# Optimization experiments

Hardware: AMD Instinct MI355X
Metric: run time of the kernel (lower is better)

The kernel has to match this reference:

```python
import jax, jax.numpy as jnp
import numpy as np

T, KBLK, EMB, B = 2048, 64, 512, 4


def _make_coords(t, k):
    # head1: for each j, cols = block_start(j) + arange(j % k + 1)  (block-causal local)
    j = np.arange(t)
    cnt1 = (j % k) + 1
    rows1 = np.repeat(j, cnt1)
    off1 = np.arange(cnt1.sum()) - np.repeat(np.cumsum(cnt1) - cnt1, cnt1)
    cols1 = (rows1 // k) * k + off1
    # head2: for each block start c, rows = arange(c, t), col = c  (strided block-start)
    starts = np.arange(t // k) * k
    cnt2 = t - starts
    base = np.repeat(starts, cnt2)
    off2 = np.arange(cnt2.sum()) - np.repeat(np.cumsum(cnt2) - cnt2, cnt2)
    rows2, cols2 = base + off2, base
    c1 = np.stack([rows1, cols1], 1).astype(np.int32)
    c2 = np.stack([rows2, cols2], 1).astype(np.int32)
    return c1, c2


def setup_inputs() -> dict:
    key = jax.random.key(0)
    ks = jax.random.split(key, 6)
    s = 1.0 / float(np.sqrt(EMB))
    c1, c2 = _make_coords(T, KBLK)
    return {
        "x": jax.random.normal(ks[0], (B, T, EMB), jnp.float32),
        "Wk": jax.random.normal(ks[1], (EMB, EMB), jnp.float32) * s,
        "bk": jnp.zeros((EMB,), jnp.float32),
        "Wq": jax.random.normal(ks[2], (EMB, EMB), jnp.float32) * s,
        "bq": jnp.zeros((EMB,), jnp.float32),
        "Wv": jax.random.normal(ks[3], (EMB, EMB), jnp.float32) * s,
        "bv": jnp.zeros((EMB,), jnp.float32),
        "Wu": jax.random.normal(ks[4], (EMB, 2 * EMB), jnp.float32) * s,
        "bu": jnp.zeros((EMB,), jnp.float32),
        "coords1": jnp.asarray(c1),
        "coords2": jnp.asarray(c2),
    }


def _sparse_head(Kt, Qt, Vt, coords):
    rows, cols = coords[:, 0], coords[:, 1]
    # dot[b,p] = (K @ Q^T)[b, rows[p], cols[p]] = K[b,rows[p],:] . Q[b,cols[p],:]
    dot = jnp.einsum('bpe,bpe->bp', Kt[:, rows], Qt[:, cols])
    # sparse.batchmm: out[b,r] = sum_{p: rows[p]=r} dot[b,p] * V[b, cols[p]]
    out = jnp.zeros_like(Vt).at[:, rows].add(dot[..., None] * Vt[:, cols])
    return out


def reference(x, Wk, bk, Wq, bq, Wv, bv, Wu, bu, coords1, coords2):
    Kt = x @ Wk.T + bk
    Qt = x @ Wq.T + bq
    Vt = x @ Wv.T + bv
    h1 = _sparse_head(Kt, Qt, Vt, coords1)
    h2 = _sparse_head(Kt, Qt, Vt, coords2)
    comb = jnp.concatenate([h1, h2], axis=-1)  # [B, T, 2*EMB]
    return comb @ Wu.T + bu
```

## Files before the change

kernel.cpp:

```cpp
#include <hip/hip_runtime.h>


typedef unsigned short u16;
typedef __attribute__((ext_vector_type(8))) short short8;
typedef __attribute__((ext_vector_type(4))) float f32x4;

constexpr int TDIM  = 2048;
constexpr int EMB_D = 512;
constexpr int BB    = 4;
constexpr int NBLK  = 32;
constexpr int LDK   = 1536;

__device__ __forceinline__ u16 f2b(float f) {
    unsigned u = __float_as_uint(f);
    unsigned r = (u + 0x7FFFu + ((u >> 16) & 1u)) >> 16;
    return (u16)r;
}

__global__ __launch_bounds__(256) void prep_k(
    const float* __restrict__ x, const float* __restrict__ Wk, const float* __restrict__ Wq,
    const float* __restrict__ Wv, const float* __restrict__ Wu,
    const float* __restrict__ bk, const float* __restrict__ bq, const float* __restrict__ bv,
    u16* __restrict__ xb, u16* __restrict__ wcat, u16* __restrict__ wvtb,
    u16* __restrict__ wub, float* __restrict__ biascat)
{
    const int bid = blockIdx.x, tid = threadIdx.x;
    if (bid < 5120) {
        const float* src; u16* dst; int base;
        if (bid < 4096)      { src = x;  dst = xb;            base = bid * 1024; }
        else if (bid < 4352) { src = Wk; dst = wcat;          base = (bid - 4096) * 1024; }
        else if (bid < 4608) { src = Wq; dst = wcat + 262144; base = (bid - 4352) * 1024; }
        else                 { src = Wu; dst = wub;           base = (bid - 4608) * 1024; }
        const int idx = base + tid * 4;
        float4 v = *(const float4*)(src + idx);
        ushort4 o = { f2b(v.x), f2b(v.y), f2b(v.z), f2b(v.w) };
        *(ushort4*)(dst + idx) = o;
    } else if (bid < 5184) {
        __shared__ float T[64][65];
        const int t = bid - 5120;
        const int j0 = (t >> 3) * 64, k0 = (t & 7) * 64;
        const int rr = tid >> 4, c4 = (tid & 15) * 4;
        #pragma unroll
        for (int it = 0; it < 4; ++it) {
            const int j = rr + it * 16;
            float4 v = *(const float4*)(Wv + (size_t)(j0 + j) * 512 + k0 + c4);
            T[c4+0][j] = v.x; T[c4+1][j] = v.y; T[c4+2][j] = v.z; T[c4+3][j] = v.w;
        }
        __syncthreads();
        #pragma unroll
        for (int it = 0; it < 4; ++it) {
            const int k = rr + it * 16;
            ushort4 o = { f2b(T[k][c4+0]), f2b(T[k][c4+1]), f2b(T[k][c4+2]), f2b(T[k][c4+3]) };
            *(ushort4*)(wvtb + (size_t)(k0 + k) * 512 + j0 + c4) = o;
        }
    } else if (bid < 5200) {
        const int o = (bid - 5184) * 64 + (tid >> 2);
        const int p = tid & 3;
        const int n = o & 511, half = o >> 9;
        const float* wr = Wu + (size_t)n * 1024 + half * 512 + p * 128;
        const float* br = bv + p * 128;
        float s = 0.f;
        #pragma unroll
        for (int j = 0; j < 128; j += 4) {
            float4 a = *(const float4*)(wr + j);
            float4 b = *(const float4*)(br + j);
            s += a.x*b.x + a.y*b.y + a.z*b.z + a.w*b.w;
        }
        s += __shfl_xor(s, 1);
        s += __shfl_xor(s, 2);
        if (p == 0) biascat[1024 + o] = s;
    } else {
        const int idx = tid * 4;
        float4 v = (idx < 512) ? *(const float4*)(bk + idx)
                               : *(const float4*)(bq + idx - 512);
        *(float4*)(biascat + idx) = v;
    }
}

__global__ __launch_bounds__(256) void wc_gemm_k(
    const u16* __restrict__ wub, const u16* __restrict__ wvtb, u16* __restrict__ wcat)
{
    __shared__ u16 As[128 * 32];
    __shared__ u16 Bs[128 * 32];
    const int bm = blockIdx.x * 128;
    const int bn = blockIdx.y * 128;
    const int tid  = threadIdx.x;
    const int wid  = tid >> 6;
    const int lane = tid & 63;
    const int l15  = lane & 15;
    const int quad = lane >> 4;
    const int wm = (wid & 1) * 64;
    const int wn = (wid >> 1) * 64;
    f32x4 acc[4][4] = {};
    const int srow  = tid >> 2;
    const int skoff = (tid & 3) * 8;
    const int m0 = bm + srow, m1 = bm + 64 + srow;
    const u16* Ag0 = wub + (size_t)(m0 & 511) * 1024 + (m0 >> 9) * 512 + skoff;
    const u16* Ag1 = wub + (size_t)(m1 & 511) * 1024 + (m1 >> 9) * 512 + skoff;
    const u16* Bg  = wvtb + (size_t)(bn + srow) * 512 + skoff;
    char* AsBase = (char*)As + wid * 1024;
    char* BsBase = (char*)Bs + wid * 1024;

    for (int k0 = 0; k0 < 512; k0 += 32) {
        __syncthreads();
        __builtin_amdgcn_global_load_lds(
            (const __attribute__((address_space(1))) void*)(Ag0 + k0),
            (__attribute__((address_space(3))) void*)AsBase, 16, 0, 0);
        __builtin_amdgcn_global_load_lds(
            (const __attribute__((address_space(1))) void*)(Ag1 + k0),
            (__attribute__((address_space(3))) void*)(AsBase + 4096), 16, 0, 0);
        __builtin_amdgcn_global_load_lds(
            (const __attribute__((address_space(1))) void*)(Bg + k0),
            (__attribute__((address_space(3))) void*)BsBase, 16, 0, 0);
        __builtin_amdgcn_global_load_lds(
            (const __attribute__((address_space(1))) void*)(Bg + (size_t)64 * 512 + k0),
            (__attribute__((address_space(3))) void*)(BsBase + 4096), 16, 0, 0);
        __syncthreads();

        short8 a[4], b[4];
        #pragma unroll
        for (int i = 0; i < 4; ++i)
            a[i] = *(const short8*)((const short*)As + (wm + 16*i + l15) * 32 + quad * 8);
        #pragma unroll
        for (int j = 0; j < 4; ++j)
            b[j] = *(const short8*)((const short*)Bs + (wn + 16*j + l15) * 32 + quad * 8);
        #pragma unroll
        for (int i = 0; i < 4; ++i)
            #pragma unroll
            for (int j = 0; j < 4; ++j)
                acc[i][j] = __builtin_amdgcn_mfma_f32_16x16x32_bf16(a[i], b[j], acc[i][j], 0, 0, 0);
    }
    #pragma unroll
    for (int i = 0; i < 4; ++i)
        #pragma unroll
        for (int j = 0; j < 4; ++j) {
            const int col = bn + wn + 16*j + l15;
            #pragma unroll
            for (int r = 0; r < 4; ++r) {
                const int row = bm + wm + 16*i + quad*4 + r;
                wcat[(size_t)(1024 + row) * 512 + col] = f2b(acc[i][j][r]);
            }
        }
}

__global__ __launch_bounds__(256) void kqv_k(
    const u16* __restrict__ xb, const u16* __restrict__ wcat,
    const float* __restrict__ biascat, u16* __restrict__ KQV, u16* __restrict__ vu2sel)
{
    __shared__ u16 As[128 * 32];
    __shared__ u16 Bs[128 * 32];
    const int tid  = threadIdx.x;
    const int wid  = tid >> 6;
    const int lane = tid & 63;
    const int l15  = lane & 15;
    const int quad = lane >> 4;
    const int wm = (wid & 1) * 64;
    const int wn = (wid >> 1) * 64;
    const int srow  = tid >> 2;
    const int skoff = (tid & 3) * 8;
    char* AsBase = (char*)As + wid * 1024;
    char* BsBase = (char*)Bs + wid * 1024;
    f32x4 acc[4][4] = {};

    const bool sel = (blockIdx.x == 64);
    if (sel && blockIdx.y >= 4) return;

    const u16 *Ag0, *Ag1, *Bg;
    const int bn = blockIdx.y * 128;
    if (!sel) {
        const int bm = blockIdx.x * 128;
        Ag0 = xb + (size_t)(bm + srow) * EMB_D + skoff;
        Ag1 = Ag0 + (size_t)64 * EMB_D;
        Bg  = wcat + (size_t)(bn + srow) * EMB_D + skoff;
    } else {
        const int r0 = srow, r1 = srow + 64;
        const int g0 = (r0 >> 5) * TDIM + (r0 & 31) * 64;
        const int g1 = (r1 >> 5) * TDIM + (r1 & 31) * 64;
        Ag0 = xb + (size_t)g0 * EMB_D + skoff;
        Ag1 = xb + (size_t)g1 * EMB_D + skoff;
        Bg  = wcat + (size_t)(1536 + bn + srow) * EMB_D + skoff;
    }

    for (int k0 = 0; k0 < EMB_D; k0 += 32) {
        __syncthreads();
        __builtin_amdgcn_global_load_lds(
            (const __attribute__((address_space(1))) void*)(Ag0 + k0),
            (__attribute__((address_space(3))) void*)AsBase, 16, 0, 0);
        __builtin_amdgcn_global_load_lds(
            (const __attribute__((address_space(1))) void*)(Ag1 + k0),
            (__attribute__((address_space(3))) void*)(AsBase + 4096), 16, 0, 0);
        __builtin_amdgcn_global_load_lds(
            (const __attribute__((address_space(1))) void*)(Bg + k0),
            (__attribute__((address_space(3))) void*)BsBase, 16, 0, 0);
        __builtin_amdgcn_global_load_lds(
            (const __attribute__((address_space(1))) void*)(Bg + (size_t)64 * EMB_D + k0),
            (__attribute__((address_space(3))) void*)(BsBase + 4096), 16, 0, 0);
        __syncthreads();

        short8 a[4], b[4];
        #pragma unroll
        for (int i = 0; i < 4; ++i)
            a[i] = *(const short8*)((const short*)As + (wm + 16*i + l15) * 32 + quad * 8);
        #pragma unroll
        for (int j = 0; j < 4; ++j)
            b[j] = *(const short8*)((const short*)Bs + (wn + 16*j + l15) * 32 + quad * 8);
        #pragma unroll
        for (int i = 0; i < 4; ++i)
            #pragma unroll
            for (int j = 0; j < 4; ++j)
                acc[i][j] = __builtin_amdgcn_mfma_f32_16x16x32_bf16(a[i], b[j], acc[i][j], 0, 0, 0);
    }

    if (!sel) {
        const int bm = blockIdx.x * 128;
        #pragma unroll
        for (int i = 0; i < 4; ++i)
            #pragma unroll
            for (int j = 0; j < 4; ++j) {
                const int col = bn + wn + 16*j + l15;
                const float bvv = biascat[col];
                #pragma unroll
                for (int r = 0; r < 4; ++r) {
                    const int row = bm + wm + 16*i + quad*4 + r;
                    KQV[(size_t)row * LDK + col] = f2b(acc[i][j][r] + bvv);
                }
            }
    } else {
        #pragma unroll
        for (int i = 0; i < 4; ++i)
            #pragma unroll
            for (int j = 0; j < 4; ++j) {
                const int col = bn + wn + 16*j + l15;
                const float bvv = biascat[1536 + col];
                #pragma unroll
                for (int r = 0; r < 4; ++r) {
                    const int row = wm + 16*i + quad*4 + r;
                    vu2sel[(size_t)row * 512 + col] = f2b(acc[i][j][r] + bvv);
                }
            }
    }
}

__global__ __launch_bounds__(256) void heads_k(
    const u16* __restrict__ KQV, const u16* __restrict__ vu2sel,
    const float* __restrict__ bu, float* __restrict__ out)
{
    __shared__ u16 smA[64 * 104];
    __shared__ u16 smVT[128 * 104];
    __shared__ u16 pK[2][64 * 32];
    __shared__ u16 pQ[2][64 * 32];
    __shared__ u16 pQs[2][32 * 32];

    const int blk = blockIdx.x, b = blockIdx.y;
    const int e0 = blockIdx.z * 128;
    const int tid = threadIdx.x;
    const int wid = tid >> 6, lane = tid & 63;
    const int l15 = lane & 15, quad = lane >> 4;
    const size_t row0 = (size_t)b * TDIM + (size_t)blk * 64;
    const size_t brow = (size_t)b * TDIM;
    const int srow_base = 16 * wid + quad * 4;

    #pragma unroll
    for (int it = 0; it < 4; ++it) {
        const int id = tid + 256 * it;
        const int c  = id & 63;
        const int eo = (id >> 6) * 8;
        short8 v = *(const short8*)(KQV + (row0 + c) * (size_t)LDK + 1024 + e0 + eo);
        #pragma unroll
        for (int i = 0; i < 8; ++i) smVT[(eo + i) * 104 + c] = (u16)v[i];
    }
    #pragma unroll
    for (int it = 0; it < 2; ++it) {
        const int id = tid + 256 * it;
        const int m  = id & 31;
        const int eo = (id >> 5) * 8;
        short8 v = *(const short8*)(vu2sel + ((size_t)(b * 32 + m)) * 512 + e0 + eo);
        #pragma unroll
        for (int i = 0; i < 8; ++i) smVT[(eo + i) * 104 + 64 + m] = (u16)v[i];
    }

    f32x4 s1[4] = {}; f32x4 s2[2] = {};
    const int srow  = tid >> 2;
    const int skoff = (tid & 3) * 8;
    const int qsrow = srow & 31;
    const int qsp   = tid >> 7;
    const u16* Kg  = KQV + (row0 + srow) * (size_t)LDK + skoff;
    const u16* Qg  = KQV + (row0 + srow) * (size_t)LDK + 512 + skoff;
    const u16* Qsg = KQV + (brow + (size_t)64 * qsrow) * (size_t)LDK + 512 + qsp * 32 + skoff;
    char* dK  = (char*)pK  + wid * 1024;
    char* dQ  = (char*)pQ  + wid * 1024;
    char* dQs = (char*)pQs + wid * 1024;

    for (int k0 = 0; k0 < 512; k0 += 64) {
        __syncthreads();
        __builtin_amdgcn_global_load_lds(
            (const __attribute__((address_space(1))) void*)(Kg + k0),
            (__attribute__((address_space(3))) void*)dK, 16, 0, 0);
        __builtin_amdgcn_global_load_lds(
            (const __attribute__((address_space(1))) void*)(Kg + k0 + 32),
            (__attribute__((address_space(3))) void*)(dK + 4096), 16, 0, 0);
        __builtin_amdgcn_global_load_lds(
            (const __attribute__((address_space(1))) void*)(Qg + k0),
            (__attribute__((address_space(3))) void*)dQ, 16, 0, 0);
        __builtin_amdgcn_global_load_lds(
            (const __attribute__((address_space(1))) void*)(Qg + k0 + 32),
            (__attribute__((address_space(3))) void*)(dQ + 4096), 16, 0, 0);
        __builtin_amdgcn_global_load_lds(
            (const __attribute__((address_space(1))) void*)(Qsg + k0),
            (__attribute__((address_space(3))) void*)dQs, 16, 0, 0);
        __syncthreads();

        short8 a0 = *(const short8*)(pK[0] + (16 * wid + l15) * 32 + quad * 8);
        short8 a1 = *(const short8*)(pK[1] + (16 * wid + l15) * 32 + quad * 8);
        #pragma unroll
        for (int j = 0; j < 4; ++j) {
            short8 b0 = *(const short8*)(pQ[0] + (16 * j + l15) * 32 + quad * 8);
            short8 b1 = *(const short8*)(pQ[1] + (16 * j + l15) * 32 + quad * 8);
            s1[j] = __builtin_amdgcn_mfma_f32_16x16x32_bf16(a0, b0, s1[j], 0, 0, 0);
            s1[j] = __builtin_amdgcn_mfma_f32_16x16x32_bf16(a1, b1, s1[j], 0, 0, 0);
        }
        #pragma unroll
        for (int j = 0; j < 2; ++j) {
            short8 b0 = *(const short8*)(pQs[0] + (16 * j + l15) * 32 + quad * 8);
            short8 b1 = *(const short8*)(pQs[1] + (16 * j + l15) * 32 + quad * 8);
            s2[j] = __builtin_amdgcn_mfma_f32_16x16x32_bf16(a0, b0, s2[j], 0, 0, 0);
            s2[j] = __builtin_amdgcn_mfma_f32_16x16x32_bf16(a1, b1, s2[j], 0, 0, 0);
        }
    }

    #pragma unroll
    for (int j = 0; j < 4; ++j)
        #pragma unroll
        for (int r = 0; r < 4; ++r) {
            const int rr = srow_base + r;
            const int cc = 16 * j + l15;
            smA[rr * 104 + cc] = f2b((cc <= rr) ? s1[j][r] : 0.0f);
        }
    #pragma unroll
    for (int j = 0; j < 2; ++j)
        #pragma unroll
        for (int r = 0; r < 4; ++r) {
            const int m  = 16 * j + l15;
            const int rr = srow_base + r;
            smA[rr * 104 + 64 + m] = f2b((m <= blk) ? s2[j][r] : 0.0f);
        }
    __syncthreads();

    f32x4 o[8] = {};
    const u16* arow = smA + (16 * wid + l15) * 104;
    #pragma unroll
    for (int ks = 0; ks < 3; ++ks) {
        short8 as = *(const short8*)(arow + 32 * ks + quad * 8);
        #pragma unroll
        for (int nt = 0; nt < 8; ++nt) {
            short8 bs = *(const short8*)(smVT + (16 * nt + l15) * 104 + 32 * ks + quad * 8);
            o[nt] = __builtin_amdgcn_mfma_f32_16x16x32_bf16(as, bs, o[nt], 0, 0, 0);
        }
    }
    #pragma unroll
    for (int nt = 0; nt < 8; ++nt) {
        const int col = e0 + 16 * nt + l15;
        const float bvv = bu[col];
        #pragma unroll
        for (int r = 0; r < 4; ++r)
            out[(row0 + srow_base + r) * (size_t)EMB_D + col] = o[nt][r] + bvv;
    }
}

extern "C" void kernel_launch(void* const* d_in, const int* in_sizes, int n_in,
                              void* d_out, int out_size, void* d_ws, size_t ws_size,
                              hipStream_t stream)
{
    const float* x  = (const float*)d_in[0];
    const float* Wk = (const float*)d_in[1];
    const float* bk = (const float*)d_in[2];
    const float* Wq = (const float*)d_in[3];
    const float* bq = (const float*)d_in[4];
    const float* Wv = (const float*)d_in[5];
    const float* bv = (const float*)d_in[6];
    const float* Wu = (const float*)d_in[7];
    const float* bu = (const float*)d_in[8];
    float* out = (float*)d_out;

    char* w = (char*)d_ws;
    u16*   KQV     = (u16*)  (w + ((size_t)0  << 20));
    u16*   xb      = (u16*)  (w + ((size_t)24 << 20));
    u16*   wcat    = (u16*)  (w + ((size_t)32 << 20));
    u16*   vu2sel  = (u16*)  (w + ((size_t)34 << 20));
    u16*   wvtb    = (u16*)  (w + ((size_t)35 << 20));
    u16*   wub     = (u16*)  (w + ((size_t)36 << 20));
    float* biascat = (float*)(w + ((size_t)37 << 20));

    dim3 blk(256);
    hipLaunchKernelGGL(prep_k, dim3(5201), blk, 0, stream,
                       x, Wk, Wq, Wv, Wu, bk, bq, bv, xb, wcat, wvtb, wub, biascat);
    hipLaunchKernelGGL(wc_gemm_k, dim3(8, 4), blk, 0, stream, wub, wvtb, wcat);
    hipLaunchKernelGGL(kqv_k, dim3(65, 12), blk, 0, stream,
                       xb, wcat, biascat, KQV, vu2sel);
    hipLaunchKernelGGL(heads_k, dim3(NBLK, BB, 4), blk, 0, stream,
                       KQV, vu2sel, bu, out);
}
```

Measured before the change: 150.0 us.

## Widen heads kernel to 512 threads, split score work across waves, halve z-grid

The heads kernel now runs 512-thread blocks over a z-grid of 2 instead of 4, so each block covers 256 output columns in two passes of 128. The score phase is split so waves 0-3 compute the local block scores and waves 4-7 compute the strided block-start scores, each wave loading half of the K chunk. This halves how often the score GEMM is recomputed per row block and spreads its work over more waves. In exchange, the V tile is reloaded between the two output passes with extra barriers, and the grid has fewer blocks (256), which could leave CUs idle.

Result: no change. 152.5 us (+1.7%).

```diff
diff --git a/kernel.cpp b/kernel.cpp
--- a/kernel.cpp
+++ b/kernel.cpp
@@ -241,7 +241,7 @@
     }
 }
 
-__global__ __launch_bounds__(256) void heads_k(
+__global__ __launch_bounds__(512) void heads_k(
     const u16* __restrict__ KQV, const u16* __restrict__ vu2sel,
     const float* __restrict__ bu, float* __restrict__ out)
 {
@@ -251,45 +251,50 @@
     __shared__ u16 pQ[2][64 * 32];
     __shared__ u16 pQs[2][32 * 32];
 
-    const int blk = blockIdx.x, b = blockIdx.y;
-    const int e0 = blockIdx.z * 128;
+    const int blk = blockIdx.x, b = blockIdx.y, z = blockIdx.z;
     const int tid = threadIdx.x;
     const int wid = tid >> 6, lane = tid & 63;
     const int l15 = lane & 15, quad = lane >> 4;
     const size_t row0 = (size_t)b * TDIM + (size_t)blk * 64;
     const size_t brow = (size_t)b * TDIM;
-    const int srow_base = 16 * wid + quad * 4;
-
-    #pragma unroll
-    for (int it = 0; it < 4; ++it) {
-        const int id = tid + 256 * it;
-        const int c  = id & 63;
-        const int eo = (id >> 6) * 8;
-        short8 v = *(const short8*)(KQV + (row0 + c) * (size_t)LDK + 1024 + e0 + eo);
-        #pragma unroll
-        for (int i = 0; i < 8; ++i) smVT[(eo + i) * 104 + c] = (u16)v[i];
-    }
-    #pragma unroll
-    for (int it = 0; it < 2; ++it) {
-        const int id = tid + 256 * it;
-        const int m  = id & 31;
-        const int eo = (id >> 5) * 8;
-        short8 v = *(const short8*)(vu2sel + ((size_t)(b * 32 + m)) * 512 + e0 + eo);
-        #pragma unroll
-        for (int i = 0; i < 8; ++i) smVT[(eo + i) * 104 + 64 + m] = (u16)v[i];
-    }
-
-    f32x4 s1[4] = {}; f32x4 s2[2] = {};
-    const int srow  = tid >> 2;
-    const int skoff = (tid & 3) * 8;
-    const int qsrow = srow & 31;
-    const int qsp   = tid >> 7;
-    const u16* Kg  = KQV + (row0 + srow) * (size_t)LDK + skoff;
-    const u16* Qg  = KQV + (row0 + srow) * (size_t)LDK + 512 + skoff;
+    const int ebase = z * 256;
+
+    {
+        const int ec0 = ebase;
+        #pragma unroll
+        for (int it = 0; it < 2; ++it) {
+            const int id = tid + 512 * it;
+            const int c  = id & 63;
+            const int eo = (id >> 6) * 8;
+            short8 v = *(const short8*)(KQV + (row0 + c) * (size_t)LDK + 1024 + ec0 + eo);
+            #pragma unroll
+            for (int i = 0; i < 8; ++i) smVT[(eo + i) * 104 + c] = (u16)v[i];
+        }
+        {
+            const int m  = tid & 31;
+            const int eo = (tid >> 5) * 8;
+            short8 v = *(const short8*)(vu2sel + ((size_t)(b * 32 + m)) * 512 + ec0 + eo);
+            #pragma unroll
+            for (int i = 0; i < 8; ++i) smVT[(eo + i) * 104 + 64 + m] = (u16)v[i];
+        }
+    }
+
+    f32x4 s[4] = {};
+    const int h      = tid >> 8;
+    const int hrow   = (tid & 255) >> 2;
+    const int skoff  = (tid & 3) * 8;
+    const u16* Kg  = KQV + (row0 + hrow) * (size_t)LDK + h * 32 + skoff;
+    const u16* Qg  = KQV + (row0 + hrow) * (size_t)LDK + 512 + h * 32 + skoff;
+    const int qsrow = hrow & 31;
+    const int qsp   = (tid & 255) >> 7;
     const u16* Qsg = KQV + (brow + (size_t)64 * qsrow) * (size_t)LDK + 512 + qsp * 32 + skoff;
-    char* dK  = (char*)pK  + wid * 1024;
-    char* dQ  = (char*)pQ  + wid * 1024;
-    char* dQs = (char*)pQs + wid * 1024;
+    char* dK  = (char*)pK  + h * 4096 + (wid & 3) * 1024;
+    char* dQ  = (char*)pQ  + h * 4096 + (wid & 3) * 1024;
+    char* dQs = (char*)pQs + (wid & 3) * 1024;
+
+    const bool isS1 = (wid < 4);
+    const int strip = wid & 3;
+    const int arow_off = (strip * 16 + l15) * 32 + quad * 8;
 
     for (int k0 = 0; k0 < 512; k0 += 64) {
         __syncthreads();
@@ -297,73 +302,102 @@
             (const __attribute__((address_space(1))) void*)(Kg + k0),
             (__attribute__((address_space(3))) void*)dK, 16, 0, 0);
         __builtin_amdgcn_global_load_lds(
-            (const __attribute__((address_space(1))) void*)(Kg + k0 + 32),
-            (__attribute__((address_space(3))) void*)(dK + 4096), 16, 0, 0);
-        __builtin_amdgcn_global_load_lds(
             (const __attribute__((address_space(1))) void*)(Qg + k0),
             (__attribute__((address_space(3))) void*)dQ, 16, 0, 0);
-        __builtin_amdgcn_global_load_lds(
-            (const __attribute__((address_space(1))) void*)(Qg + k0 + 32),
-            (__attribute__((address_space(3))) void*)(dQ + 4096), 16, 0, 0);
-        __builtin_amdgcn_global_load_lds(
-            (const __attribute__((address_space(1))) void*)(Qsg + k0),
-            (__attribute__((address_space(3))) void*)dQs, 16, 0, 0);
-        __syncthreads();
-
-        short8 a0 = *(const short8*)(pK[0] + (16 * wid + l15) * 32 + quad * 8);
-        short8 a1 = *(const short8*)(pK[1] + (16 * wid + l15) * 32 + quad * 8);
-        #pragma unroll
-        for (int j = 0; j < 4; ++j) {
-            short8 b0 = *(const short8*)(pQ[0] + (16 * j + l15) * 32 + quad * 8);
-            short8 b1 = *(const short8*)(pQ[1] + (16 * j + l15) * 32 + quad * 8);
-            s1[j] = __builtin_amdgcn_mfma_f32_16x16x32_bf16(a0, b0, s1[j], 0, 0, 0);
-            s1[j] = __builtin_amdgcn_mfma_f32_16x16x32_bf16(a1, b1, s1[j], 0, 0, 0);
-        }
-        #pragma unroll
-        for (int j = 0; j < 2; ++j) {
-            short8 b0 = *(const short8*)(pQs[0] + (16 * j + l15) * 32 + quad * 8);
-            short8 b1 = *(const short8*)(pQs[1] + (16 * j + l15) * 32 + quad * 8);
-            s2[j] = __builtin_amdgcn_mfma_f32_16x16x32_bf16(a0, b0, s2[j], 0, 0, 0);
-            s2[j] = __builtin_amdgcn_mfma_f32_16x16x32_bf16(a1, b1, s2[j], 0, 0, 0);
-        }
-    }
-
-    #pragma unroll
-    for (int j = 0; j < 4; ++j)
-        #pragma unroll
-        for (int r = 0; r < 4; ++r) {
-            const int rr = srow_base + r;
-            const int cc = 16 * j + l15;
-            smA[rr * 104 + cc] = f2b((cc <= rr) ? s1[j][r] : 0.0f);
-        }
-    #pragma unroll
-    for (int j = 0; j < 2; ++j)
-        #pragma unroll
-        for (int r = 0; r < 4; ++r) {
-            const int m  = 16 * j + l15;
-            const int rr = srow_base + r;
-            smA[rr * 104 + 64 + m] = f2b((m <= blk) ? s2[j][r] : 0.0f);
-        }
+        if (tid < 256)
+            __builtin_amdgcn_global_load_lds(
+                (const __attribute__((address_space(1))) void*)(Qsg + k0),
+                (__attribute__((address_space(3))) void*)dQs, 16, 0, 0);
+        __syncthreads();
+
+        short8 a0 = *(const short8*)(pK[0] + arow_off);
+        short8 a1 = *(const short8*)(pK[1] + arow_off);
+        if (isS1) {
+            #pragma unroll
+            for (int j = 0; j < 4; ++j) {
+                short8 b0 = *(const short8*)(pQ[0] + (16 * j + l15) * 32 + quad * 8);
+                short8 b1 = *(const short8*)(pQ[1] + (16 * j + l15) * 32 + quad * 8);
+                s[j] = __builtin_amdgcn_mfma_f32_16x16x32_bf16(a0, b0, s[j], 0, 0, 0);
+                s[j] = __builtin_amdgcn_mfma_f32_16x16x32_bf16(a1, b1, s[j], 0, 0, 0);
+            }
+        } else {
+            #pragma unroll
+            for (int j = 0; j < 2; ++j) {
+                short8 b0 = *(const short8*)(pQs[0] + (16 * j + l15) * 32 + quad * 8);
+                short8 b1 = *(const short8*)(pQs[1] + (16 * j + l15) * 32 + quad * 8);
+                s[j] = __builtin_amdgcn_mfma_f32_16x16x32_bf16(a0, b0, s[j], 0, 0, 0);
+                s[j] = __builtin_amdgcn_mfma_f32_16x16x32_bf16(a1, b1, s[j], 0, 0, 0);
+            }
+        }
+    }
+
+    {
+        const int rbase = strip * 16 + quad * 4;
+        if (isS1) {
+            #pragma unroll
+            for (int j = 0; j < 4; ++j)
+                #pragma unroll
+                for (int r = 0; r < 4; ++r) {
+                    const int rr = rbase + r;
+                    const int cc = 16 * j + l15;
+                    smA[rr * 104 + cc] = f2b((cc <= rr) ? s[j][r] : 0.0f);
+                }
+        } else {
+            #pragma unroll
+            for (int j = 0; j < 2; ++j)
+                #pragma unroll
+                for (int r = 0; r < 4; ++r) {
+                    const int m  = 16 * j + l15;
+                    const int rr = rbase + r;
+                    smA[rr * 104 + 64 + m] = f2b((m <= blk) ? s[j][r] : 0.0f);
+                }
+        }
+    }
     __syncthreads();
 
-    f32x4 o[8] = {};
-    const u16* arow = smA + (16 * wid + l15) * 104;
-    #pragma unroll
-    for (int ks = 0; ks < 3; ++ks) {
-        short8 as = *(const short8*)(arow + 32 * ks + quad * 8);
-        #pragma unroll
-        for (int nt = 0; nt < 8; ++nt) {
-            short8 bs = *(const short8*)(smVT + (16 * nt + l15) * 104 + 32 * ks + quad * 8);
-            o[nt] = __builtin_amdgcn_mfma_f32_16x16x32_bf16(as, bs, o[nt], 0, 0, 0);
-        }
-    }
-    #pragma unroll
-    for (int nt = 0; nt < 8; ++nt) {
-        const int col = e0 + 16 * nt + l15;
-        const float bvv = bu[col];
-        #pragma unroll
-        for (int r = 0; r < 4; ++r)
-            out[(row0 + srow_base + r) * (size_t)EMB_D + col] = o[nt][r] + bvv;
+    const int rbase = (wid & 3) * 16;
+    const int chalf = (wid >> 2) * 64;
+    const u16* arow = smA + (rbase + l15) * 104;
+    for (int p = 0; p < 2; ++p) {
+        if (p == 1) {
+            __syncthreads();
+            const int ec0 = ebase + 128;
+            #pragma unroll
+            for (int it = 0; it < 2; ++it) {
+                const int id = tid + 512 * it;
+                const int c  = id & 63;
+                const int eo = (id >> 6) * 8;
+                short8 v = *(const short8*)(KQV + (row0 + c) * (size_t)LDK + 1024 + ec0 + eo);
+                #pragma unroll
+                for (int i = 0; i < 8; ++i) smVT[(eo + i) * 104 + c] = (u16)v[i];
+            }
+            {
+                const int m  = tid & 31;
+                const int eo = (tid >> 5) * 8;
+                short8 v = *(const short8*)(vu2sel + ((size_t)(b * 32 + m)) * 512 + ec0 + eo);
+                #pragma unroll
+                for (int i = 0; i < 8; ++i) smVT[(eo + i) * 104 + 64 + m] = (u16)v[i];
+            }
+            __syncthreads();
+        }
+        f32x4 o[4] = {};
+        #pragma unroll
+        for (int ks = 0; ks < 3; ++ks) {
+            short8 as = *(const short8*)(arow + 32 * ks + quad * 8);
+            #pragma unroll
+            for (int nt = 0; nt < 4; ++nt) {
+                short8 bs = *(const short8*)(smVT + (chalf + 16 * nt + l15) * 104 + 32 * ks + quad * 8);
+                o[nt] = __builtin_amdgcn_mfma_f32_16x16x32_bf16(as, bs, o[nt], 0, 0, 0);
+            }
+        }
+        #pragma unroll
+        for (int nt = 0; nt < 4; ++nt) {
+            const int col = ebase + p * 128 + chalf + 16 * nt + l15;
+            const float bvv = bu[col];
+            #pragma unroll
+            for (int r = 0; r < 4; ++r)
+                out[(row0 + rbase + quad * 4 + r) * (size_t)EMB_D + col] = o[nt][r] + bvv;
+        }
     }
 }
 
@@ -397,6 +431,6 @@
     hipLaunchKernelGGL(wc_gemm_k, dim3(8, 4), blk, 0, stream, wub, wvtb, wcat);
     hipLaunchKernelGGL(kqv_k, dim3(65, 12), blk, 0, stream,
                        xb, wcat, biascat, KQV, vu2sel);
-    hipLaunchKernelGGL(heads_k, dim3(NBLK, BB, 4), blk, 0, stream,
+    hipLaunchKernelGGL(heads_k, dim3(NBLK, BB, 2), dim3(512), 0, stream,
                        KQV, vu2sel, bu, out);
 }
```
